# Kernel tuning notes

Measured on AMD Instinct MI355X. Metric: run time of the kernel, lower is better.

The kernel has to match this reference:

```python
import jax, jax.numpy as jnp
import numpy as np
from jax.scipy.special import logsumexp

WORD_DIM = 512
SCRF_DIM = 256
N_TAGS = 12
ALLOWED_SPAN = 8
START_ID = 10
STOP_ID = 11
SEQ_LEN = 768
N_SPANS = 96


def _compute_scores(h, Wl, bl, Wr, br, Gl, bgl, Gr, bgr, Wt, bt, transitions):
    # h: [1, L, D] already projected by Dense
    Lc, D = h.shape[1], h.shape[2]
    scores = jnp.zeros((1, Lc, Lc, D), h.dtype)
    diag = jnp.arange(Lc)
    ht = h
    scores = scores.at[:, diag, diag].set(ht)
    for sl in range(1, min(ALLOWED_SPAN, Lc)):
        l, r = ht[:, :-1], ht[:, 1:]
        h_hat = 4.0 * jax.nn.sigmoid(l @ Wl.T + bl + r @ Wr.T + br) - 2.0
        # exp/normalize over 3 gates == softmax over gate axis
        g = (l @ Gl.T + bgl + r @ Gr.T + bgr).reshape(1, Lc - sl, 3, D)
        wgt = jax.nn.softmax(g, axis=2)
        ht = wgt[:, :, 0] * h_hat + wgt[:, :, 1] * l + wgt[:, :, 2] * r
        scores = scores.at[:, diag[:Lc - sl], diag[sl:]].set(ht)
    tagsc = scores @ Wt.T + bt  # [1, L, L, T]
    # final[b,i,j,prev,tag] = tagsc[b,i,j,tag] + transitions[prev,tag]
    return tagsc[:, :, :, None, :] + transitions[None, None, None]


def _forward_pass(s5):
    # s5: [1, L, L, T, T]; semi-Markov forward algorithm, windows of width <= ALLOWED_SPAN
    Lc, T = s5.shape[1], s5.shape[3]
    A = ALLOWED_SPAN
    i0 = jnp.arange(1, Lc + 1)
    k = jnp.arange(A)
    p = i0[:, None] - A + k[None, :]              # candidate span-start positions [L, A]
    m = p >= 0                                    # valid window mask (istarts = max(0, i-A))
    x = s5[0][jnp.clip(p, 0), (i0 - 1)[:, None]]  # [L, A, T, T] span scores ending at i-1
    buf0 = jnp.full((A, T), -10000.0, s5.dtype).at[A - 1, START_ID].set(0.0)

    def step(buf, inp):
        xi, mi = inp
        # tmp[k, prev, tag] = score + logalpha[start, prev]
        tmp = jnp.where(mi[:, None, None], xi + buf[:, :, None], -1e30)
        na = logsumexp(tmp, axis=(0, 1))  # [T]
        return jnp.concatenate([buf[1:], na[None]], axis=0), na

    _, alphas = jax.lax.scan(step, buf0, (x, m))
    return alphas[-1, :STOP_ID].sum()


def _gold_score(s5, tags):
    Lc, T = s5.shape[1], s5.shape[3]
    gf = tags[:, :, 0] * (Lc * T * T) + tags[:, :, 1] * (T * T) + tags[:, :, 2] * T + tags[:, :, 3]
    return jnp.take_along_axis(s5.reshape(1, -1), gf, axis=1).sum()


def setup_inputs() -> dict:
    key = jax.random.key(0)
    ks = jax.random.split(key, 16)
    D, W3 = SCRF_DIM, 3 * SCRF_DIM
    s = 0.05
    def w(k, shape):
        return jax.random.normal(k, shape, dtype=jnp.float32) * s
    return {
        "feats": jax.random.normal(ks[0], (1, SEQ_LEN, WORD_DIM), dtype=jnp.float32),
        "tags": jax.random.randint(ks[1], (1, N_SPANS, 4), 0, N_TAGS),
        "Wd": w(ks[2], (D, WORD_DIM)), "bd": jnp.zeros((D,), jnp.float32),
        "Wl": w(ks[3], (D, D)), "bl": jnp.zeros((D,), jnp.float32),
        "Wr": w(ks[4], (D, D)), "br": jnp.zeros((D,), jnp.float32),
        "Gl": w(ks[5], (W3, D)), "bgl": jnp.zeros((W3,), jnp.float32),
        "Gr": w(ks[6], (W3, D)), "bgr": jnp.zeros((W3,), jnp.float32),
        "Wt": w(ks[7], (N_TAGS, D)), "bt": jnp.zeros((N_TAGS,), jnp.float32),
        "transitions": w(ks[8], (N_TAGS, N_TAGS)),
    }


def reference(feats, tags, Wd, bd, Wl, bl, Wr, br, Gl, bgl, Gr, bgr, Wt, bt, transitions):
    h = feats @ Wd.T + bd  # Dense: word_dim -> scrf_dim
    s5 = _compute_scores(h, Wl, bl, Wr, br, Gl, bgl, Gr, bgr, Wt, bt, transitions)
    gold = _gold_score(s5, tags)
    logZ = _forward_pass(s5)
    return logZ - gold
```

## Files before the change

### kernel.cpp

```cpp
#include <hip/hip_runtime.h>

typedef __attribute__((ext_vector_type(8))) short short8;
typedef __attribute__((ext_vector_type(4))) float f32x4;

__device__ __forceinline__ float bf2f(short s) {
  return __uint_as_float(((unsigned)(unsigned short)s) << 16);
}
__device__ __forceinline__ unsigned short f2bf(float f) {
  unsigned u = __float_as_uint(f);
  unsigned rounding = 0x7fffu + ((u >> 16) & 1u);
  return (unsigned short)((u + rounding) >> 16);
}

__global__ void prep_kernel(const float* __restrict__ feats, const float* __restrict__ Wd,
                            const float* __restrict__ Wl, const float* __restrict__ Wr,
                            const float* __restrict__ Gl, const float* __restrict__ Gr,
                            const float* __restrict__ bl, const float* __restrict__ br,
                            const float* __restrict__ bgl, const float* __restrict__ bgr,
                            unsigned short* __restrict__ featsB, unsigned short* __restrict__ WdB,
                            unsigned short* __restrict__ WcB, float* __restrict__ bc)
{
  int idx = blockIdx.x * 256 + threadIdx.x;
  if (idx < 393216) {
    featsB[idx] = f2bf(feats[idx]);
  } else if (idx < 524288) {
    int j = idx - 393216;
    WdB[j] = f2bf(Wd[j]);
  } else if (idx < 1048576) {
    int j = idx - 524288;
    int o = j >> 9, k = j & 511;
    float v;
    if (k < 256) v = (o < 256) ? Wl[o*256 + k] : Gl[(o-256)*256 + k];
    else { int k2 = k - 256; v = (o < 256) ? Wr[o*256 + k2] : Gr[(o-256)*256 + k2]; }
    WcB[j] = f2bf(v);
  } else if (idx < 1049600) {
    int o = idx - 1048576;
    bc[o] = (o < 256) ? bl[o] + br[o] : bgl[o-256] + bgr[o-256];
  }
}

__global__ __launch_bounds__(256) void hgemm_kernel(const unsigned short* __restrict__ A,
                                                    const unsigned short* __restrict__ W,
                                                    const float* __restrict__ bd,
                                                    unsigned short* __restrict__ C)
{
  __shared__ __align__(16) unsigned short As[64][72];
  __shared__ __align__(16) unsigned short Ws[64][72];
  int p0 = blockIdx.x * 64;
  int n0 = blockIdx.y * 64;
  int tid = threadIdx.x;
  int wave = tid >> 6, lane = tid & 63;
  f32x4 acc[4];
  #pragma unroll
  for (int i = 0; i < 4; ++i)
    #pragma unroll
    for (int j = 0; j < 4; ++j) acc[i][j] = 0.f;

  int lr = tid >> 3;
  int c8 = (tid & 7) * 8;
  for (int kt = 0; kt < 8; ++kt) {
    int kb = kt * 64;
    #pragma unroll
    for (int rr = 0; rr < 64; rr += 32) {
      int row = lr + rr;
      *(short8*)(&As[row][c8]) = *(const short8*)(A + (size_t)(p0 + row)*512 + kb + c8);
      *(short8*)(&Ws[row][c8]) = *(const short8*)(W + (size_t)(n0 + row)*512 + kb + c8);
    }
    __syncthreads();
    int q8 = (lane >> 4) * 8;
    #pragma unroll
    for (int kk = 0; kk < 2; ++kk) {
      short8 b = *(const short8*)(&Ws[wave*16 + (lane & 15)][kk*32 + q8]);
      #pragma unroll
      for (int mt = 0; mt < 4; ++mt) {
        short8 a = *(const short8*)(&As[mt*16 + (lane & 15)][kk*32 + q8]);
        acc[mt] = __builtin_amdgcn_mfma_f32_16x16x32_bf16(a, b, acc[mt], 0, 0, 0);
      }
    }
    __syncthreads();
  }
  int o = n0 + wave*16 + (lane & 15);
  float bias = bd[o];
  #pragma unroll
  for (int mt = 0; mt < 4; ++mt)
    #pragma unroll
    for (int r = 0; r < 4; ++r) {
      int row = p0 + mt*16 + (lane >> 4)*4 + r;
      C[row*256 + o] = f2bf(acc[mt][r] + bias);
    }
}

__global__ __launch_bounds__(256) void iter_kernel(const unsigned short* __restrict__ htp,
                                                   const unsigned short* __restrict__ Wc,
                                                   const float* __restrict__ bc,
                                                   unsigned short* __restrict__ htn,
                                                   int Mvalid)
{
  __shared__ __align__(16) unsigned short As[64][72];
  __shared__ __align__(16) unsigned short Ws[64][72];
  __shared__ float Cs[64][64];
  int p0 = blockIdx.x * 64;
  int n0 = blockIdx.y * 16;
  int tid = threadIdx.x;
  int wave = tid >> 6, lane = tid & 63;
  f32x4 acc[4];
  #pragma unroll
  for (int i = 0; i < 4; ++i)
    #pragma unroll
    for (int j = 0; j < 4; ++j) acc[i][j] = 0.f;

  int lr = tid >> 3;
  int c8 = (tid & 7) * 8;
  for (int kt = 0; kt < 8; ++kt) {
    int kb = kt * 64;
    int shift = kb >> 8;
    int kcol = kb & 255;
    #pragma unroll
    for (int rr = 0; rr < 64; rr += 32) {
      int row = lr + rr;
      int grow = p0 + row + shift; if (grow > 767) grow = 767;
      *(short8*)(&As[row][c8]) = *(const short8*)(htp + (size_t)grow*256 + kcol + c8);
      int o = (row >> 4)*256 + n0 + (row & 15);
      *(short8*)(&Ws[row][c8]) = *(const short8*)(Wc + (size_t)o*512 + kb + c8);
    }
    __syncthreads();
    int q8 = (lane >> 4) * 8;
    #pragma unroll
    for (int kk = 0; kk < 2; ++kk) {
      short8 b = *(const short8*)(&Ws[wave*16 + (lane & 15)][kk*32 + q8]);
      #pragma unroll
      for (int mt = 0; mt < 4; ++mt) {
        short8 a = *(const short8*)(&As[mt*16 + (lane & 15)][kk*32 + q8]);
        acc[mt] = __builtin_amdgcn_mfma_f32_16x16x32_bf16(a, b, acc[mt], 0, 0, 0);
      }
    }
    __syncthreads();
  }
  #pragma unroll
  for (int mt = 0; mt < 4; ++mt)
    #pragma unroll
    for (int r = 0; r < 4; ++r)
      Cs[mt*16 + (lane >> 4)*4 + r][wave*16 + (lane & 15)] = acc[mt][r];
  __syncthreads();

  int dl = tid & 15;
  int d = n0 + dl;
  float bz = bc[d], b0 = bc[256 + d], b1 = bc[512 + d], b2v = bc[768 + d];
  for (int pr = tid >> 4; pr < 64; pr += 16) {
    int p = p0 + pr;
    if (p >= Mvalid) continue;
    float z  = Cs[pr][dl]      + bz;
    float g0 = Cs[pr][16 + dl] + b0;
    float g1 = Cs[pr][32 + dl] + b1;
    float g2 = Cs[pr][48 + dl] + b2v;
    float l = bf2f((short)htp[p*256 + d]);
    float r = bf2f((short)htp[(p+1)*256 + d]);
    float hh = 4.f / (1.f + __expf(-z)) - 2.f;
    float mg = fmaxf(g0, fmaxf(g1, g2));
    float e0 = __expf(g0 - mg), e1 = __expf(g1 - mg), e2 = __expf(g2 - mg);
    float inv = 1.f / (e0 + e1 + e2);
    htn[p*256 + d] = f2bf((e0*hh + e1*l + e2*r) * inv);
  }
}

__global__ __launch_bounds__(128) void band_kernel(const unsigned short* __restrict__ htall,
                                                   const float* __restrict__ Wt,
                                                   const float* __restrict__ bt,
                                                   float* __restrict__ Bband,
                                                   float* __restrict__ Xn,
                                                   float* __restrict__ mu)
{
  __shared__ __align__(16) unsigned short rows[8][264];
  __shared__ float sred[96];
  __shared__ float smu;
  int i = blockIdx.x + 1;
  int tid = threadIdx.x;
  for (int q = tid; q < 256; q += 128) {
    int k = q >> 5, cc = (q & 31) * 8;
    int p = i - 8 + k, sl = 7 - k;
    short8 v;
    if (p >= 0) {
      v = *(const short8*)(htall + ((size_t)sl*768 + p)*256 + cc);
    } else {
      for (int j = 0; j < 8; ++j) v[j] = 0;
    }
    *(short8*)(&rows[k][cc]) = v;
  }
  __syncthreads();
  float res = -1e30f;
  if (tid < 96) {
    int t = tid >> 3, k = tid & 7;
    int p = i - 8 + k;
    if (p >= 0) {
      float acc = 0.f;
      for (int dch = 0; dch < 256; dch += 8) {
        float4 wa = *(const float4*)(Wt + t*256 + dch);
        float4 wb = *(const float4*)(Wt + t*256 + dch + 4);
        short8 hv = *(const short8*)(&rows[k][dch]);
        acc += wa.x*bf2f(hv[0]) + wa.y*bf2f(hv[1]) + wa.z*bf2f(hv[2]) + wa.w*bf2f(hv[3])
             + wb.x*bf2f(hv[4]) + wb.y*bf2f(hv[5]) + wb.z*bf2f(hv[6]) + wb.w*bf2f(hv[7]);
      }
      res = acc + bt[t];
    }
    Bband[(size_t)i*96 + tid] = res;
    sred[tid] = res;
  }
  __syncthreads();
  if (tid < 32) {
    float m = fmaxf(sred[tid], fmaxf(sred[tid+32], sred[tid+64]));
    #pragma unroll
    for (int off = 16; off; off >>= 1) m = fmaxf(m, __shfl_down(m, off));
    if (tid == 0) { mu[i] = m; smu = m; }
  }
  __syncthreads();
  if (tid < 96) Xn[(size_t)i*96 + tid] = __expf(res - smu);
}

__global__ __launch_bounds__(256) void chunkT_kernel(const float* __restrict__ Xn,
                                                     const float* __restrict__ mu,
                                                     const float* __restrict__ trans,
                                                     float* __restrict__ T,
                                                     float* __restrict__ C0)
{
  int chunk = blockIdx.y;
  int a = chunk * 16;
  int tid = threadIdx.x;
  if (blockIdx.x == 0 && tid == 0) C0[chunk] = 0.f;
  int wv = tid >> 6;
  int lane = tid & 63;
  int g = lane / 12;
  int t = lane - g * 12;
  int cidx = blockIdx.x * 20 + wv * 5 + g;
  bool active = (g < 5) && (cidx < 96);
  int c = active ? cidx : 95;
  int s = c / 12, tau = c - s * 12;
  float Etc[12];
  #pragma unroll
  for (int j = 0; j < 12; ++j) Etc[j] = __expf(trans[j*12 + t]);
  float NA[8], V[8];
  #pragma unroll
  for (int j = 0; j < 8; ++j) { NA[j] = 0.f; V[j] = 0.f; }
  #pragma unroll
  for (int j = 0; j < 8; ++j) if (j == s) {
    NA[j] = (t == tau) ? 1.f : 0.f;
    V[j]  = Etc[tau];
  }
  int gb = (g * 12) * 4;
  #pragma unroll
  for (int m = 1; m <= 16; ++m) {
    const float* xr = Xn + (size_t)(a + m) * 96 + t * 8;
    float4 x0 = *(const float4*)xr;
    float4 x1 = *(const float4*)(xr + 4);
    float sf = __expf(-mu[a + m]);
    float na = x0.x*V[0] + x0.y*V[1] + x0.z*V[2] + x0.w*V[3]
             + x1.x*V[4] + x1.y*V[5] + x1.z*V[6] + x1.w*V[7];
    int nai = __float_as_int(na);
    float nb[12];
    #pragma unroll
    for (int j = 0; j < 12; ++j)
      nb[j] = __int_as_float(__builtin_amdgcn_ds_bpermute(gb + j*4, nai));
    float p0 = nb[0]*Etc[0] + nb[1]*Etc[1] + nb[2]*Etc[2]  + nb[3]*Etc[3];
    float p1 = nb[4]*Etc[4] + nb[5]*Etc[5] + nb[6]*Etc[6]  + nb[7]*Etc[7];
    float p2 = nb[8]*Etc[8] + nb[9]*Etc[9] + nb[10]*Etc[10] + nb[11]*Etc[11];
    float v = (p0 + p1) + p2;
    #pragma unroll
    for (int k = 0; k < 7; ++k) { NA[k] = NA[k+1]*sf; V[k] = V[k+1]*sf; }
    NA[7] = na; V[7] = v;
  }
  if (active) {
    float* dst = T + (size_t)chunk * 9216 + c;
    #pragma unroll
    for (int j = 0; j < 8; ++j) dst[(size_t)(j*12 + t) * 96] = NA[j];
  }
}

#define TPAD 100
__global__ __launch_bounds__(256) void treemul_kernel(const float* __restrict__ Tin,
                                                      const float* __restrict__ Cin,
                                                      float* __restrict__ Tout,
                                                      float* __restrict__ Cout)
{
  __shared__ float Bs[96 * TPAD];
  __shared__ float Acs[96 * TPAD];
  __shared__ float red[8];
  int j = blockIdx.y;
  int cs = blockIdx.x * 48;
  const float* Ag = Tin + (size_t)(2*j) * 9216;
  const float* Bg = Tin + (size_t)(2*j + 1) * 9216;
  int tid = threadIdx.x;
  int wv = tid >> 6, lane = tid & 63;

  float4 av[9], bv[9];
  const float* ap = Ag + tid * 36;
  const float* bp = Bg + tid * 36;
  #pragma unroll
  for (int q = 0; q < 9; ++q) av[q] = *(const float4*)(ap + q*4);
  #pragma unroll
  for (int q = 0; q < 9; ++q) bv[q] = *(const float4*)(bp + q*4);
  float ma = 0.f, mb = 0.f;
  #pragma unroll
  for (int q = 0; q < 9; ++q) {
    ma = fmaxf(ma, fmaxf(fmaxf(av[q].x, av[q].y), fmaxf(av[q].z, av[q].w)));
    mb = fmaxf(mb, fmaxf(fmaxf(bv[q].x, bv[q].y), fmaxf(bv[q].z, bv[q].w)));
  }
  #pragma unroll
  for (int off = 32; off; off >>= 1) {
    ma = fmaxf(ma, __shfl_down(ma, off));
    mb = fmaxf(mb, __shfl_down(mb, off));
  }
  if (lane == 0) { red[wv] = ma; red[4 + wv] = mb; }
  __syncthreads();
  float fa = fmaxf(fmaxf(red[0], red[1]), fmaxf(red[2], red[3]));
  float fb = fmaxf(fmaxf(red[4], red[5]), fmaxf(red[6], red[7]));
  float ia = 1.0f / fa, ib = 1.0f / fb;

  #pragma unroll
  for (int q = 0; q < 9; ++q) {
    int e = tid*36 + q*4;
    int r = e / 96, k = e - r*96;
    float4 b = bv[q];
    b.x *= ib; b.y *= ib; b.z *= ib; b.w *= ib;
    *(float4*)&Bs[r*TPAD + k] = b;
    float4 a = av[q];
    Acs[(k+0)*TPAD + r] = a.x * ia;
    Acs[(k+1)*TPAD + r] = a.y * ia;
    Acs[(k+2)*TPAD + r] = a.z * ia;
    Acs[(k+3)*TPAD + r] = a.w * ia;
  }
  __syncthreads();

  int tr = tid >> 4, tc = tid & 15;
  int r0 = tr * 6, c0 = cs + tc * 3;
  float acc[6][3];
  #pragma unroll
  for (int i = 0; i < 6; ++i)
    #pragma unroll
    for (int m = 0; m < 3; ++m) acc[i][m] = 0.f;
  for (int k = 0; k < 96; k += 4) {
    float4 a0 = *(const float4*)&Acs[(c0+0)*TPAD + k];
    float4 a1 = *(const float4*)&Acs[(c0+1)*TPAD + k];
    float4 a2 = *(const float4*)&Acs[(c0+2)*TPAD + k];
    #pragma unroll
    for (int i = 0; i < 6; ++i) {
      float4 b = *(const float4*)&Bs[(r0+i)*TPAD + k];
      acc[i][0] += b.x*a0.x + b.y*a0.y + b.z*a0.z + b.w*a0.w;
      acc[i][1] += b.x*a1.x + b.y*a1.y + b.z*a1.z + b.w*a1.w;
      acc[i][2] += b.x*a2.x + b.y*a2.y + b.z*a2.z + b.w*a2.w;
    }
  }
  float* op = Tout + (size_t)j * 9216;
  #pragma unroll
  for (int i = 0; i < 6; ++i)
    #pragma unroll
    for (int m = 0; m < 3; ++m)
      op[(size_t)(r0+i)*96 + c0 + m] = acc[i][m];
  if (blockIdx.x == 0 && tid == 0)
    Cout[j] = Cin[2*j] + Cin[2*j + 1] + __logf(fa) + __logf(fb);
}

__global__ __launch_bounds__(256, 1) void final_kernel(const float* __restrict__ Tm,
    const float* __restrict__ Cm, const float* __restrict__ Bband,
    const float* __restrict__ mu, const float* __restrict__ trans,
    const float* __restrict__ bt, const int* __restrict__ tags,
    float* __restrict__ out)
{
  __shared__ float Qs[2][96 * TPAD];
  __shared__ float vv[4][96];
  __shared__ float red[8];
  __shared__ float redm[4];
  int tid = threadIdx.x;
  int wv = tid >> 6, lane = tid & 63;

  float4 P[9];
  const float* p0 = Tm + tid * 36;
  #pragma unroll
  for (int q = 0; q < 9; ++q) P[q] = *(const float4*)(p0 + q*4);

  float gold = 0.f;
  if (tid < 96) {
    int a = tags[tid*4+0], b = tags[tid*4+1], cc = tags[tid*4+2], d = tags[tid*4+3];
    float v = trans[cc*12 + d];
    int sl = b - a;
    if (sl >= 0 && sl < 8) v += Bband[(size_t)(b+1)*96 + d*8 + (7 - sl)];
    else v += bt[d];
    gold = v;
  }
  float mp = 0.f;
  for (int q = tid; q < 768; q += 256) mp += mu[1 + q];
  #pragma unroll
  for (int off = 32; off; off >>= 1) {
    gold += __shfl_down(gold, off);
    mp   += __shfl_down(mp, off);
  }
  if (lane == 0) { red[wv] = gold; red[4 + wv] = mp; }

  #pragma unroll
  for (int q = 0; q < 9; ++q) {
    int e = tid*36 + q*4;
    int r = e / 96, k = e - r*96;
    *(float4*)&Qs[0][r*TPAD + k] = P[q];
  }
  if (tid < 96) vv[0][tid] = (tid == 94) ? 1.f : 0.f;
  __syncthreads();
  float gold_t = red[0] + red[1] + red[2] + red[3];
  float musum  = red[4] + red[5] + red[6] + red[7];
  float Ct = Cm[0] + Cm[1] + Cm[2];

  #pragma unroll
  for (int s = 0; s < 3; ++s) {
    if (s < 2) {
      const float* pn = Tm + (size_t)(s+1)*9216 + tid*36;
      #pragma unroll
      for (int q = 0; q < 9; ++q) P[q] = *(const float4*)(pn + q*4);
    }
    float acc = 0.f;
    if (tid < 96) {
      const float* Qr = &Qs[s & 1][tid * TPAD];
      #pragma unroll
      for (int k = 0; k < 96; k += 4) {
        float4 qv = *(const float4*)(Qr + k);
        float4 zv = *(const float4*)&vv[s][k];
        acc += qv.x*zv.x + qv.y*zv.y + qv.z*zv.z + qv.w*zv.w;
      }
    }
    float am = (tid < 96) ? acc : 0.f;
    #pragma unroll
    for (int off = 32; off; off >>= 1) am = fmaxf(am, __shfl_down(am, off));
    if (lane == 0) redm[wv] = am;
    __syncthreads();
    float mx = fmaxf(fmaxf(redm[0], redm[1]), fmaxf(redm[2], redm[3]));
    Ct += __logf(mx);
    if (tid < 96) vv[s+1][tid] = acc / mx;
    if (s < 2) {
      #pragma unroll
      for (int q = 0; q < 9; ++q) {
        int e = tid*36 + q*4;
        int r = e / 96, k = e - r*96;
        *(float4*)&Qs[(s+1)&1][r*TPAD + k] = P[q];
      }
    }
    __syncthreads();
  }
  if (tid == 0) {
    float lsum = 0.f;
    #pragma unroll
    for (int t = 0; t < 11; ++t) lsum += __logf(vv[3][84 + t]);
    out[0] = lsum + 11.f * (Ct + musum) - gold_t;
  }
}

extern "C" void kernel_launch(void* const* d_in, const int* in_sizes, int n_in,
                              void* d_out, int out_size, void* d_ws, size_t ws_size,
                              hipStream_t stream)
{
  const float* feats = (const float*)d_in[0];
  const int*   tags  = (const int*)  d_in[1];
  const float* Wd    = (const float*)d_in[2];
  const float* bd    = (const float*)d_in[3];
  const float* Wl    = (const float*)d_in[4];
  const float* bl    = (const float*)d_in[5];
  const float* Wr    = (const float*)d_in[6];
  const float* br    = (const float*)d_in[7];
  const float* Gl    = (const float*)d_in[8];
  const float* bgl   = (const float*)d_in[9];
  const float* Gr    = (const float*)d_in[10];
  const float* bgr   = (const float*)d_in[11];
  const float* Wt    = (const float*)d_in[12];
  const float* bt    = (const float*)d_in[13];
  const float* trans = (const float*)d_in[14];
  float* out = (float*)d_out;

  char* ws = (char*)d_ws;
  unsigned short* featsB = (unsigned short*)(ws + 0);
  unsigned short* WdB    = (unsigned short*)(ws + 786432);
  unsigned short* WcB    = (unsigned short*)(ws + 1048576);
  float*          bc     = (float*)         (ws + 2097152);
  unsigned short* ht     = (unsigned short*)(ws + 2101248);
  float*          Bband  = (float*)         (ws + 5246976);
  float*          Xn     = (float*)         (ws + 5542272);
  float*          muv    = (float*)         (ws + 5837568);
  float*          T      = (float*)         (ws + 5841664);
  float*          Tb     = (float*)         (ws + 0);
  float*          C0     = (float*)         (ws + 1048576);
  float*          Ca     = (float*)         (ws + 1048832);
  float*          Cb     = (float*)         (ws + 1049088);

  prep_kernel<<<4100, 256, 0, stream>>>(feats, Wd, Wl, Wr, Gl, Gr, bl, br, bgl, bgr,
                                        featsB, WdB, WcB, bc);
  hgemm_kernel<<<dim3(12, 4), 256, 0, stream>>>(featsB, WdB, bd, ht);
  for (int sl = 1; sl <= 7; ++sl)
    iter_kernel<<<dim3(12, 16), 256, 0, stream>>>(ht + (size_t)(sl-1)*768*256, WcB, bc,
                                                  ht + (size_t)sl*768*256, 768 - sl);
  band_kernel<<<768, 128, 0, stream>>>(ht, Wt, bt, Bband, Xn, muv);
  chunkT_kernel<<<dim3(5, 48), 256, 0, stream>>>(Xn, muv, trans, T, C0);
  treemul_kernel<<<dim3(2, 24), 256, 0, stream>>>(T,  C0, Tb, Ca);
  treemul_kernel<<<dim3(2, 12), 256, 0, stream>>>(Tb, Ca, T,  Cb);
  treemul_kernel<<<dim3(2,  6), 256, 0, stream>>>(T,  Cb, Tb, Ca);
  treemul_kernel<<<dim3(2,  3), 256, 0, stream>>>(Tb, Ca, T,  Cb);
  final_kernel<<<1, 256, 0, stream>>>(T, Cb, Bband, muv, trans, bt, tags, out);
}
```

Baseline: 206.4 us.

## Fuse GEMM chain into cooperative kernel and merge band/chunk/tree stages

Replaces the prep, projection GEMM and seven iteration kernels with a single cooperative kernel. It converts fp32 inputs to bf16 on the fly and separates the span-length steps with grid syncs, which removes the separate conversion pass and eight launches. The band and chunk-transfer stages are merged into one kernel. The four-level tree reduction becomes two kernels that each combine four matrices, with per-matrix max scaling. The final kernel changes to two matrix-vector products. This cuts launch count and intermediate global traffic, but adds grid-sync overhead and converts the weights redundantly in every iteration.

```diff
diff --git a/kernel.cpp b/kernel.cpp
--- a/kernel.cpp
+++ b/kernel.cpp
@@ -1,4 +1,6 @@
 #include <hip/hip_runtime.h>
+#include <hip/hip_cooperative_groups.h>
+namespace cg = cooperative_groups;
 
 typedef __attribute__((ext_vector_type(8))) short short8;
 typedef __attribute__((ext_vector_type(4))) float f32x4;
@@ -11,370 +13,473 @@
   unsigned rounding = 0x7fffu + ((u >> 16) & 1u);
   return (unsigned short)((u + rounding) >> 16);
 }
-
-__global__ void prep_kernel(const float* __restrict__ feats, const float* __restrict__ Wd,
-                            const float* __restrict__ Wl, const float* __restrict__ Wr,
-                            const float* __restrict__ Gl, const float* __restrict__ Gr,
-                            const float* __restrict__ bl, const float* __restrict__ br,
-                            const float* __restrict__ bgl, const float* __restrict__ bgr,
-                            unsigned short* __restrict__ featsB, unsigned short* __restrict__ WdB,
-                            unsigned short* __restrict__ WcB, float* __restrict__ bc)
-{
-  int idx = blockIdx.x * 256 + threadIdx.x;
-  if (idx < 393216) {
-    featsB[idx] = f2bf(feats[idx]);
-  } else if (idx < 524288) {
-    int j = idx - 393216;
-    WdB[j] = f2bf(Wd[j]);
-  } else if (idx < 1048576) {
-    int j = idx - 524288;
-    int o = j >> 9, k = j & 511;
-    float v;
-    if (k < 256) v = (o < 256) ? Wl[o*256 + k] : Gl[(o-256)*256 + k];
-    else { int k2 = k - 256; v = (o < 256) ? Wr[o*256 + k2] : Gr[(o-256)*256 + k2]; }
-    WcB[j] = f2bf(v);
-  } else if (idx < 1049600) {
-    int o = idx - 1048576;
-    bc[o] = (o < 256) ? bl[o] + br[o] : bgl[o-256] + bgr[o-256];
-  }
-}
-
-__global__ __launch_bounds__(256) void hgemm_kernel(const unsigned short* __restrict__ A,
-                                                    const unsigned short* __restrict__ W,
-                                                    const float* __restrict__ bd,
-                                                    unsigned short* __restrict__ C)
-{
-  __shared__ __align__(16) unsigned short As[64][72];
-  __shared__ __align__(16) unsigned short Ws[64][72];
-  int p0 = blockIdx.x * 64;
-  int n0 = blockIdx.y * 64;
-  int tid = threadIdx.x;
-  int wave = tid >> 6, lane = tid & 63;
-  f32x4 acc[4];
-  #pragma unroll
-  for (int i = 0; i < 4; ++i)
-    #pragma unroll
-    for (int j = 0; j < 4; ++j) acc[i][j] = 0.f;
-
-  int lr = tid >> 3;
-  int c8 = (tid & 7) * 8;
-  for (int kt = 0; kt < 8; ++kt) {
-    int kb = kt * 64;
-    #pragma unroll
-    for (int rr = 0; rr < 64; rr += 32) {
-      int row = lr + rr;
-      *(short8*)(&As[row][c8]) = *(const short8*)(A + (size_t)(p0 + row)*512 + kb + c8);
-      *(short8*)(&Ws[row][c8]) = *(const short8*)(W + (size_t)(n0 + row)*512 + kb + c8);
-    }
-    __syncthreads();
-    int q8 = (lane >> 4) * 8;
-    #pragma unroll
-    for (int kk = 0; kk < 2; ++kk) {
-      short8 b = *(const short8*)(&Ws[wave*16 + (lane & 15)][kk*32 + q8]);
-      #pragma unroll
-      for (int mt = 0; mt < 4; ++mt) {
-        short8 a = *(const short8*)(&As[mt*16 + (lane & 15)][kk*32 + q8]);
-        acc[mt] = __builtin_amdgcn_mfma_f32_16x16x32_bf16(a, b, acc[mt], 0, 0, 0);
-      }
-    }
-    __syncthreads();
-  }
-  int o = n0 + wave*16 + (lane & 15);
-  float bias = bd[o];
-  #pragma unroll
-  for (int mt = 0; mt < 4; ++mt)
-    #pragma unroll
-    for (int r = 0; r < 4; ++r) {
-      int row = p0 + mt*16 + (lane >> 4)*4 + r;
-      C[row*256 + o] = f2bf(acc[mt][r] + bias);
-    }
-}
-
-__global__ __launch_bounds__(256) void iter_kernel(const unsigned short* __restrict__ htp,
-                                                   const unsigned short* __restrict__ Wc,
-                                                   const float* __restrict__ bc,
-                                                   unsigned short* __restrict__ htn,
-                                                   int Mvalid)
-{
+__device__ __forceinline__ short8 cvt8(float4 a, float4 b) {
+  short8 r;
+  r[0]=(short)f2bf(a.x); r[1]=(short)f2bf(a.y); r[2]=(short)f2bf(a.z); r[3]=(short)f2bf(a.w);
+  r[4]=(short)f2bf(b.x); r[5]=(short)f2bf(b.y); r[6]=(short)f2bf(b.z); r[7]=(short)f2bf(b.w);
+  return r;
+}
+
+__global__ __launch_bounds__(256) void gemm_chain_kernel(
+    const float* __restrict__ feats, const float* __restrict__ Wd, const float* __restrict__ bd,
+    const float* __restrict__ Wl, const float* __restrict__ bl,
+    const float* __restrict__ Wr, const float* __restrict__ br,
+    const float* __restrict__ Gl, const float* __restrict__ bgl,
+    const float* __restrict__ Gr, const float* __restrict__ bgr,
+    unsigned short* __restrict__ ht)
+{
+  cg::grid_group grid = cg::this_grid();
   __shared__ __align__(16) unsigned short As[64][72];
   __shared__ __align__(16) unsigned short Ws[64][72];
   __shared__ float Cs[64][64];
-  int p0 = blockIdx.x * 64;
-  int n0 = blockIdx.y * 16;
   int tid = threadIdx.x;
   int wave = tid >> 6, lane = tid & 63;
-  f32x4 acc[4];
-  #pragma unroll
-  for (int i = 0; i < 4; ++i)
-    #pragma unroll
-    for (int j = 0; j < 4; ++j) acc[i][j] = 0.f;
-
   int lr = tid >> 3;
   int c8 = (tid & 7) * 8;
-  for (int kt = 0; kt < 8; ++kt) {
-    int kb = kt * 64;
-    int shift = kb >> 8;
-    int kcol = kb & 255;
-    #pragma unroll
-    for (int rr = 0; rr < 64; rr += 32) {
-      int row = lr + rr;
-      int grow = p0 + row + shift; if (grow > 767) grow = 767;
-      *(short8*)(&As[row][c8]) = *(const short8*)(htp + (size_t)grow*256 + kcol + c8);
-      int o = (row >> 4)*256 + n0 + (row & 15);
-      *(short8*)(&Ws[row][c8]) = *(const short8*)(Wc + (size_t)o*512 + kb + c8);
-    }
-    __syncthreads();
-    int q8 = (lane >> 4) * 8;
-    #pragma unroll
-    for (int kk = 0; kk < 2; ++kk) {
-      short8 b = *(const short8*)(&Ws[wave*16 + (lane & 15)][kk*32 + q8]);
-      #pragma unroll
-      for (int mt = 0; mt < 4; ++mt) {
-        short8 a = *(const short8*)(&As[mt*16 + (lane & 15)][kk*32 + q8]);
-        acc[mt] = __builtin_amdgcn_mfma_f32_16x16x32_bf16(a, b, acc[mt], 0, 0, 0);
-      }
-    }
-    __syncthreads();
-  }
-  #pragma unroll
-  for (int mt = 0; mt < 4; ++mt)
-    #pragma unroll
-    for (int r = 0; r < 4; ++r)
-      Cs[mt*16 + (lane >> 4)*4 + r][wave*16 + (lane & 15)] = acc[mt][r];
-  __syncthreads();
-
+
+  if (blockIdx.x < 48) {
+    int p0 = (blockIdx.x % 12) * 64;
+    int n0 = (blockIdx.x / 12) * 64;
+    f32x4 acc[4];
+    #pragma unroll
+    for (int i = 0; i < 4; ++i)
+      #pragma unroll
+      for (int j = 0; j < 4; ++j) acc[i][j] = 0.f;
+    for (int kt = 0; kt < 8; ++kt) {
+      int kb = kt * 64;
+      #pragma unroll
+      for (int rr = 0; rr < 64; rr += 32) {
+        int row = lr + rr;
+        const float* fp = feats + (size_t)(p0 + row)*512 + kb + c8;
+        *(short8*)(&As[row][c8]) = cvt8(*(const float4*)fp, *(const float4*)(fp + 4));
+        const float* wp = Wd + (size_t)(n0 + row)*512 + kb + c8;
+        *(short8*)(&Ws[row][c8]) = cvt8(*(const float4*)wp, *(const float4*)(wp + 4));
+      }
+      __syncthreads();
+      int q8 = (lane >> 4) * 8;
+      #pragma unroll
+      for (int kk = 0; kk < 2; ++kk) {
+        short8 b = *(const short8*)(&Ws[wave*16 + (lane & 15)][kk*32 + q8]);
+        #pragma unroll
+        for (int mt = 0; mt < 4; ++mt) {
+          short8 a = *(const short8*)(&As[mt*16 + (lane & 15)][kk*32 + q8]);
+          acc[mt] = __builtin_amdgcn_mfma_f32_16x16x32_bf16(a, b, acc[mt], 0, 0, 0);
+        }
+      }
+      __syncthreads();
+    }
+    int o = n0 + wave*16 + (lane & 15);
+    float bias = bd[o];
+    #pragma unroll
+    for (int mt = 0; mt < 4; ++mt)
+      #pragma unroll
+      for (int r = 0; r < 4; ++r) {
+        int row = p0 + mt*16 + (lane >> 4)*4 + r;
+        ht[(size_t)row*256 + o] = f2bf(acc[mt][r] + bias);
+      }
+  }
+  __threadfence();
+  grid.sync();
+
+  int p0 = (blockIdx.x % 12) * 64;
+  int n0 = (blockIdx.x / 12) * 16;
   int dl = tid & 15;
   int d = n0 + dl;
-  float bz = bc[d], b0 = bc[256 + d], b1 = bc[512 + d], b2v = bc[768 + d];
-  for (int pr = tid >> 4; pr < 64; pr += 16) {
-    int p = p0 + pr;
-    if (p >= Mvalid) continue;
-    float z  = Cs[pr][dl]      + bz;
-    float g0 = Cs[pr][16 + dl] + b0;
-    float g1 = Cs[pr][32 + dl] + b1;
-    float g2 = Cs[pr][48 + dl] + b2v;
-    float l = bf2f((short)htp[p*256 + d]);
-    float r = bf2f((short)htp[(p+1)*256 + d]);
-    float hh = 4.f / (1.f + __expf(-z)) - 2.f;
-    float mg = fmaxf(g0, fmaxf(g1, g2));
-    float e0 = __expf(g0 - mg), e1 = __expf(g1 - mg), e2 = __expf(g2 - mg);
-    float inv = 1.f / (e0 + e1 + e2);
-    htn[p*256 + d] = f2bf((e0*hh + e1*l + e2*r) * inv);
-  }
-}
-
-__global__ __launch_bounds__(128) void band_kernel(const unsigned short* __restrict__ htall,
-                                                   const float* __restrict__ Wt,
-                                                   const float* __restrict__ bt,
-                                                   float* __restrict__ Bband,
-                                                   float* __restrict__ Xn,
-                                                   float* __restrict__ mu)
-{
-  __shared__ __align__(16) unsigned short rows[8][264];
-  __shared__ float sred[96];
-  __shared__ float smu;
-  int i = blockIdx.x + 1;
+  float bz  = bl[d] + br[d];
+  float b0  = bgl[d] + bgr[d];
+  float b1  = bgl[256 + d] + bgr[256 + d];
+  float b2v = bgl[512 + d] + bgr[512 + d];
+
+  for (int sl = 1; sl <= 7; ++sl) {
+    const unsigned short* htp = ht + (size_t)(sl-1)*196608;
+    unsigned short* htn = ht + (size_t)sl*196608;
+    int Mvalid = 768 - sl;
+    f32x4 acc[4];
+    #pragma unroll
+    for (int i = 0; i < 4; ++i)
+      #pragma unroll
+      for (int j = 0; j < 4; ++j) acc[i][j] = 0.f;
+    for (int kt = 0; kt < 8; ++kt) {
+      int kb = kt * 64;
+      int shift = kb >> 8;
+      int kcol = kb & 255;
+      #pragma unroll
+      for (int rr = 0; rr < 64; rr += 32) {
+        int row = lr + rr;
+        int grow = p0 + row + shift; if (grow > 767) grow = 767;
+        *(short8*)(&As[row][c8]) = *(const short8*)(htp + (size_t)grow*256 + kcol + c8);
+        int seg = row >> 4;
+        int orow = n0 + (row & 15);
+        const float* wsrc;
+        if (kt < 4) wsrc = (seg == 0) ? (Wl + (size_t)orow*256 + kb + c8)
+                                      : (Gl + ((size_t)(seg-1)*256 + orow)*256 + kb + c8);
+        else        wsrc = (seg == 0) ? (Wr + (size_t)orow*256 + (kb - 256) + c8)
+                                      : (Gr + ((size_t)(seg-1)*256 + orow)*256 + (kb - 256) + c8);
+        *(short8*)(&Ws[row][c8]) = cvt8(*(const float4*)wsrc, *(const float4*)(wsrc + 4));
+      }
+      __syncthreads();
+      int q8 = (lane >> 4) * 8;
+      #pragma unroll
+      for (int kk = 0; kk < 2; ++kk) {
+        short8 b = *(const short8*)(&Ws[wave*16 + (lane & 15)][kk*32 + q8]);
+        #pragma unroll
+        for (int mt = 0; mt < 4; ++mt) {
+          short8 a = *(const short8*)(&As[mt*16 + (lane & 15)][kk*32 + q8]);
+          acc[mt] = __builtin_amdgcn_mfma_f32_16x16x32_bf16(a, b, acc[mt], 0, 0, 0);
+        }
+      }
+      __syncthreads();
+    }
+    #pragma unroll
+    for (int mt = 0; mt < 4; ++mt)
+      #pragma unroll
+      for (int r = 0; r < 4; ++r)
+        Cs[mt*16 + (lane >> 4)*4 + r][wave*16 + (lane & 15)] = acc[mt][r];
+    __syncthreads();
+    for (int pr = tid >> 4; pr < 64; pr += 16) {
+      int p = p0 + pr;
+      if (p < Mvalid) {
+        float z  = Cs[pr][dl]      + bz;
+        float g0 = Cs[pr][16 + dl] + b0;
+        float g1 = Cs[pr][32 + dl] + b1;
+        float g2 = Cs[pr][48 + dl] + b2v;
+        float l = bf2f((short)htp[(size_t)p*256 + d]);
+        float r = bf2f((short)htp[(size_t)(p+1)*256 + d]);
+        float hh = 4.f / (1.f + __expf(-z)) - 2.f;
+        float mg = fmaxf(g0, fmaxf(g1, g2));
+        float e0 = __expf(g0 - mg), e1 = __expf(g1 - mg), e2 = __expf(g2 - mg);
+        htn[(size_t)p*256 + d] = f2bf((e0*hh + e1*l + e2*r) / (e0 + e1 + e2));
+      }
+    }
+    __threadfence();
+    grid.sync();
+  }
+}
+
+#define HPAD 264
+__global__ __launch_bounds__(256) void bandchunk_kernel(
+    const unsigned short* __restrict__ htall, const float* __restrict__ Wt,
+    const float* __restrict__ bt, const float* __restrict__ trans,
+    float* __restrict__ Bband, float* __restrict__ mug,
+    float* __restrict__ T, float* __restrict__ Tmax)
+{
+  __shared__ __align__(16) unsigned short hrow[8][16][HPAD];
+  __shared__ __align__(16) float Wts[3072];
+  __shared__ float Bls[16][100];
+  __shared__ float Xls[16][100];
+  __shared__ float muls[16], sfs[16];
+  __shared__ float redmax[4];
+  int c = blockIdx.x;
+  int a = c * 16;
   int tid = threadIdx.x;
-  for (int q = tid; q < 256; q += 128) {
-    int k = q >> 5, cc = (q & 31) * 8;
-    int p = i - 8 + k, sl = 7 - k;
+
+  for (int q = tid; q < 4096; q += 256) {
+    int sl = q >> 9;
+    int rem = q & 511;
+    int j = rem >> 5;
+    int cc = (rem & 31) * 8;
+    int p = a - sl + j;
     short8 v;
-    if (p >= 0) {
-      v = *(const short8*)(htall + ((size_t)sl*768 + p)*256 + cc);
-    } else {
-      for (int j = 0; j < 8; ++j) v[j] = 0;
-    }
-    *(short8*)(&rows[k][cc]) = v;
-  }
-  __syncthreads();
-  float res = -1e30f;
-  if (tid < 96) {
-    int t = tid >> 3, k = tid & 7;
-    int p = i - 8 + k;
+    if (p >= 0) v = *(const short8*)(htall + ((size_t)sl*768 + p)*256 + cc);
+    else { for (int x = 0; x < 8; ++x) v[x] = 0; }
+    *(short8*)(&hrow[sl][j][cc]) = v;
+  }
+  for (int q = tid; q < 3072; q += 256) Wts[q] = Wt[q];
+  __syncthreads();
+
+  #pragma unroll
+  for (int rep = 0; rep < 6; ++rep) {
+    int idx = rep * 256 + tid;
+    int j = idx / 96, col = idx - j * 96;
+    int t = col >> 3, k = col & 7, sl = 7 - k;
+    int p = a - sl + j;
+    float res = -1e30f;
     if (p >= 0) {
       float acc = 0.f;
+      const unsigned short* hr = &hrow[sl][j][0];
+      const float* wr = &Wts[t * 256];
       for (int dch = 0; dch < 256; dch += 8) {
-        float4 wa = *(const float4*)(Wt + t*256 + dch);
-        float4 wb = *(const float4*)(Wt + t*256 + dch + 4);
-        short8 hv = *(const short8*)(&rows[k][dch]);
+        short8 hv = *(const short8*)(hr + dch);
+        float4 wa = *(const float4*)(wr + dch);
+        float4 wb = *(const float4*)(wr + dch + 4);
         acc += wa.x*bf2f(hv[0]) + wa.y*bf2f(hv[1]) + wa.z*bf2f(hv[2]) + wa.w*bf2f(hv[3])
              + wb.x*bf2f(hv[4]) + wb.y*bf2f(hv[5]) + wb.z*bf2f(hv[6]) + wb.w*bf2f(hv[7]);
       }
       res = acc + bt[t];
     }
-    Bband[(size_t)i*96 + tid] = res;
-    sred[tid] = res;
-  }
-  __syncthreads();
-  if (tid < 32) {
-    float m = fmaxf(sred[tid], fmaxf(sred[tid+32], sred[tid+64]));
-    #pragma unroll
-    for (int off = 16; off; off >>= 1) m = fmaxf(m, __shfl_down(m, off));
-    if (tid == 0) { mu[i] = m; smu = m; }
-  }
-  __syncthreads();
-  if (tid < 96) Xn[(size_t)i*96 + tid] = __expf(res - smu);
-}
-
-__global__ __launch_bounds__(256) void chunkT_kernel(const float* __restrict__ Xn,
-                                                     const float* __restrict__ mu,
-                                                     const float* __restrict__ trans,
-                                                     float* __restrict__ T,
-                                                     float* __restrict__ C0)
-{
-  int chunk = blockIdx.y;
-  int a = chunk * 16;
-  int tid = threadIdx.x;
-  if (blockIdx.x == 0 && tid == 0) C0[chunk] = 0.f;
-  int wv = tid >> 6;
-  int lane = tid & 63;
+    Bls[j][col] = res;
+  }
+  __syncthreads();
+  if (tid < 16) {
+    float m = -1e30f;
+    for (int col = 0; col < 96; ++col) m = fmaxf(m, Bls[tid][col]);
+    muls[tid] = m;
+    sfs[tid] = __expf(-m);
+    mug[a + 1 + tid] = m;
+  }
+  __syncthreads();
+  #pragma unroll
+  for (int rep = 0; rep < 6; ++rep) {
+    int idx = rep * 256 + tid;
+    int j = idx / 96, col = idx - j * 96;
+    float b = Bls[j][col];
+    Bband[(size_t)(a + 1 + j) * 96 + col] = b;
+    Xls[j][col] = __expf(b - muls[j]);
+  }
+  __syncthreads();
+
+  int wv = tid >> 6, lane = tid & 63;
   int g = lane / 12;
   int t = lane - g * 12;
-  int cidx = blockIdx.x * 20 + wv * 5 + g;
-  bool active = (g < 5) && (cidx < 96);
-  int c = active ? cidx : 95;
-  int s = c / 12, tau = c - s * 12;
   float Etc[12];
   #pragma unroll
   for (int j = 0; j < 12; ++j) Etc[j] = __expf(trans[j*12 + t]);
-  float NA[8], V[8];
-  #pragma unroll
-  for (int j = 0; j < 8; ++j) { NA[j] = 0.f; V[j] = 0.f; }
-  #pragma unroll
-  for (int j = 0; j < 8; ++j) if (j == s) {
-    NA[j] = (t == tau) ? 1.f : 0.f;
-    V[j]  = Etc[tau];
-  }
   int gb = (g * 12) * 4;
-  #pragma unroll
-  for (int m = 1; m <= 16; ++m) {
-    const float* xr = Xn + (size_t)(a + m) * 96 + t * 8;
-    float4 x0 = *(const float4*)xr;
-    float4 x1 = *(const float4*)(xr + 4);
-    float sf = __expf(-mu[a + m]);
-    float na = x0.x*V[0] + x0.y*V[1] + x0.z*V[2] + x0.w*V[3]
-             + x1.x*V[4] + x1.y*V[5] + x1.z*V[6] + x1.w*V[7];
-    int nai = __float_as_int(na);
-    float nb[12];
-    #pragma unroll
-    for (int j = 0; j < 12; ++j)
-      nb[j] = __int_as_float(__builtin_amdgcn_ds_bpermute(gb + j*4, nai));
-    float p0 = nb[0]*Etc[0] + nb[1]*Etc[1] + nb[2]*Etc[2]  + nb[3]*Etc[3];
-    float p1 = nb[4]*Etc[4] + nb[5]*Etc[5] + nb[6]*Etc[6]  + nb[7]*Etc[7];
-    float p2 = nb[8]*Etc[8] + nb[9]*Etc[9] + nb[10]*Etc[10] + nb[11]*Etc[11];
-    float v = (p0 + p1) + p2;
-    #pragma unroll
-    for (int k = 0; k < 7; ++k) { NA[k] = NA[k+1]*sf; V[k] = V[k+1]*sf; }
-    NA[7] = na; V[7] = v;
-  }
-  if (active) {
-    float* dst = T + (size_t)chunk * 9216 + c;
-    #pragma unroll
-    for (int j = 0; j < 8; ++j) dst[(size_t)(j*12 + t) * 96] = NA[j];
-  }
-}
-
-#define TPAD 100
-__global__ __launch_bounds__(256) void treemul_kernel(const float* __restrict__ Tin,
-                                                      const float* __restrict__ Cin,
-                                                      float* __restrict__ Tout,
-                                                      float* __restrict__ Cout)
-{
-  __shared__ float Bs[96 * TPAD];
-  __shared__ float Acs[96 * TPAD];
-  __shared__ float red[8];
-  int j = blockIdx.y;
-  int cs = blockIdx.x * 48;
-  const float* Ag = Tin + (size_t)(2*j) * 9216;
-  const float* Bg = Tin + (size_t)(2*j + 1) * 9216;
+  float tmax = 0.f;
+  for (int pass = 0; pass < 5; ++pass) {
+    int cidx = pass * 20 + wv * 5 + g;
+    bool act = (g < 5) && (cidx < 96);
+    int cc2 = act ? cidx : 95;
+    int s = cc2 / 12, tau = cc2 - s * 12;
+    float NA[8], V[8];
+    #pragma unroll
+    for (int j = 0; j < 8; ++j) { NA[j] = 0.f; V[j] = 0.f; }
+    #pragma unroll
+    for (int j = 0; j < 8; ++j) if (j == s) {
+      NA[j] = (t == tau) ? 1.f : 0.f;
+      V[j]  = Etc[tau];
+    }
+    #pragma unroll
+    for (int m = 1; m <= 16; ++m) {
+      int jj = m - 1;
+      const float* xr = &Xls[jj][t * 8];
+      float4 x0 = *(const float4*)xr;
+      float4 x1 = *(const float4*)(xr + 4);
+      float sf = sfs[jj];
+      float na = x0.x*V[0] + x0.y*V[1] + x0.z*V[2] + x0.w*V[3]
+               + x1.x*V[4] + x1.y*V[5] + x1.z*V[6] + x1.w*V[7];
+      int nai = __float_as_int(na);
+      float nb[12];
+      #pragma unroll
+      for (int j = 0; j < 12; ++j)
+        nb[j] = __int_as_float(__builtin_amdgcn_ds_bpermute(gb + j*4, nai));
+      float p0 = nb[0]*Etc[0] + nb[1]*Etc[1] + nb[2]*Etc[2]  + nb[3]*Etc[3];
+      float p1 = nb[4]*Etc[4] + nb[5]*Etc[5] + nb[6]*Etc[6]  + nb[7]*Etc[7];
+      float p2 = nb[8]*Etc[8] + nb[9]*Etc[9] + nb[10]*Etc[10] + nb[11]*Etc[11];
+      float v = (p0 + p1) + p2;
+      #pragma unroll
+      for (int k = 0; k < 7; ++k) { NA[k] = NA[k+1]*sf; V[k] = V[k+1]*sf; }
+      NA[7] = na; V[7] = v;
+    }
+    if (act) {
+      float* dst = T + (size_t)c * 9216 + cidx;
+      #pragma unroll
+      for (int j = 0; j < 8; ++j) {
+        dst[(size_t)(j*12 + t) * 96] = NA[j];
+        tmax = fmaxf(tmax, NA[j]);
+      }
+    }
+  }
+  #pragma unroll
+  for (int off = 32; off; off >>= 1) tmax = fmaxf(tmax, __shfl_down(tmax, off));
+  if (lane == 0) redmax[wv] = tmax;
+  __syncthreads();
+  if (tid == 0)
+    Tmax[c] = fmaxf(fmaxf(fmaxf(redmax[0], redmax[1]), fmaxf(redmax[2], redmax[3])), 1e-30f);
+}
+
+#define TP 100
+__device__ __forceinline__ void mm_acc(const float* __restrict__ Bs,
+                                       const float* __restrict__ Ain,
+                                       int r0, int cl0, float acc[6][3])
+{
+  #pragma unroll
+  for (int i = 0; i < 6; ++i)
+    #pragma unroll
+    for (int m = 0; m < 3; ++m) acc[i][m] = 0.f;
+  for (int k = 0; k < 96; k += 4) {
+    float4 a0 = *(const float4*)(Ain + (cl0+0)*TP + k);
+    float4 a1 = *(const float4*)(Ain + (cl0+1)*TP + k);
+    float4 a2 = *(const float4*)(Ain + (cl0+2)*TP + k);
+    #pragma unroll
+    for (int i = 0; i < 6; ++i) {
+      float4 b = *(const float4*)(Bs + (r0+i)*TP + k);
+      acc[i][0] += b.x*a0.x + b.y*a0.y + b.z*a0.z + b.w*a0.w;
+      acc[i][1] += b.x*a1.x + b.y*a1.y + b.z*a1.z + b.w*a1.w;
+      acc[i][2] += b.x*a2.x + b.y*a2.y + b.z*a2.z + b.w*a2.w;
+    }
+  }
+}
+
+__global__ __launch_bounds__(256) void tree1_kernel(const float* __restrict__ Tin,
+    const float* __restrict__ Tmax, float* __restrict__ Tout,
+    float* __restrict__ TmaxO, float* __restrict__ Cout)
+{
+  __shared__ float Bs[96 * TP];
+  __shared__ float Rt[2][48 * TP];
+  __shared__ float redm[4];
+  int j = blockIdx.x >> 1, slice = blockIdx.x & 1;
+  int c0 = slice * 48;
   int tid = threadIdx.x;
-  int wv = tid >> 6, lane = tid & 63;
-
-  float4 av[9], bv[9];
-  const float* ap = Ag + tid * 36;
-  const float* bp = Bg + tid * 36;
-  #pragma unroll
-  for (int q = 0; q < 9; ++q) av[q] = *(const float4*)(ap + q*4);
-  #pragma unroll
-  for (int q = 0; q < 9; ++q) bv[q] = *(const float4*)(bp + q*4);
-  float ma = 0.f, mb = 0.f;
-  #pragma unroll
-  for (int q = 0; q < 9; ++q) {
-    ma = fmaxf(ma, fmaxf(fmaxf(av[q].x, av[q].y), fmaxf(av[q].z, av[q].w)));
-    mb = fmaxf(mb, fmaxf(fmaxf(bv[q].x, bv[q].y), fmaxf(bv[q].z, bv[q].w)));
-  }
-  #pragma unroll
-  for (int off = 32; off; off >>= 1) {
-    ma = fmaxf(ma, __shfl_down(ma, off));
-    mb = fmaxf(mb, __shfl_down(mb, off));
-  }
-  if (lane == 0) { red[wv] = ma; red[4 + wv] = mb; }
-  __syncthreads();
-  float fa = fmaxf(fmaxf(red[0], red[1]), fmaxf(red[2], red[3]));
-  float fb = fmaxf(fmaxf(red[4], red[5]), fmaxf(red[6], red[7]));
-  float ia = 1.0f / fa, ib = 1.0f / fb;
-
+  const float* M0 = Tin + (size_t)(4*j    ) * 9216;
+  const float* M1 = Tin + (size_t)(4*j + 1) * 9216;
+  const float* M2 = Tin + (size_t)(4*j + 2) * 9216;
+  const float* M3 = Tin + (size_t)(4*j + 3) * 9216;
+  float m0 = Tmax[4*j], m1 = Tmax[4*j+1], m2 = Tmax[4*j+2], m3 = Tmax[4*j+3];
+  float i0 = 1.f/m0, i1 = 1.f/m1, i2 = 1.f/m2, i3 = 1.f/m3;
+
+  for (int q = tid; q < 4608; q += 256) {
+    int k = q / 48, cc = q - k*48;
+    Rt[0][cc*TP + k] = M0[(size_t)k*96 + c0 + cc] * i0;
+  }
+  for (int q = tid; q < 9216; q += 256) {
+    int r = q / 96, k = q - r*96;
+    Bs[r*TP + k] = M1[q] * i1;
+  }
+  __syncthreads();
+  int r0 = (tid >> 4) * 6, cl0 = (tid & 15) * 3;
+  float acc[6][3];
+  float4 p[9];
+  #pragma unroll
+  for (int q = 0; q < 9; ++q) p[q] = *(const float4*)(M2 + tid*36 + q*4);
+  mm_acc(Bs, Rt[0], r0, cl0, acc);
+  #pragma unroll
+  for (int i = 0; i < 6; ++i)
+    #pragma unroll
+    for (int m = 0; m < 3; ++m) Rt[1][(cl0+m)*TP + (r0+i)] = acc[i][m];
+  __syncthreads();
   #pragma unroll
   for (int q = 0; q < 9; ++q) {
     int e = tid*36 + q*4;
     int r = e / 96, k = e - r*96;
-    float4 b = bv[q];
-    b.x *= ib; b.y *= ib; b.z *= ib; b.w *= ib;
-    *(float4*)&Bs[r*TPAD + k] = b;
-    float4 a = av[q];
-    Acs[(k+0)*TPAD + r] = a.x * ia;
-    Acs[(k+1)*TPAD + r] = a.y * ia;
-    Acs[(k+2)*TPAD + r] = a.z * ia;
-    Acs[(k+3)*TPAD + r] = a.w * ia;
-  }
-  __syncthreads();
-
-  int tr = tid >> 4, tc = tid & 15;
-  int r0 = tr * 6, c0 = cs + tc * 3;
+    float4 v = p[q]; v.x *= i2; v.y *= i2; v.z *= i2; v.w *= i2;
+    *(float4*)&Bs[r*TP + k] = v;
+  }
+  #pragma unroll
+  for (int q = 0; q < 9; ++q) p[q] = *(const float4*)(M3 + tid*36 + q*4);
+  __syncthreads();
+  mm_acc(Bs, Rt[1], r0, cl0, acc);
+  #pragma unroll
+  for (int i = 0; i < 6; ++i)
+    #pragma unroll
+    for (int m = 0; m < 3; ++m) Rt[0][(cl0+m)*TP + (r0+i)] = acc[i][m];
+  __syncthreads();
+  #pragma unroll
+  for (int q = 0; q < 9; ++q) {
+    int e = tid*36 + q*4;
+    int r = e / 96, k = e - r*96;
+    float4 v = p[q]; v.x *= i3; v.y *= i3; v.z *= i3; v.w *= i3;
+    *(float4*)&Bs[r*TP + k] = v;
+  }
+  __syncthreads();
+  mm_acc(Bs, Rt[0], r0, cl0, acc);
+  float* op = Tout + (size_t)j * 9216;
+  float mx = 0.f;
+  #pragma unroll
+  for (int i = 0; i < 6; ++i)
+    #pragma unroll
+    for (int m = 0; m < 3; ++m) {
+      float v = acc[i][m];
+      op[(size_t)(r0+i)*96 + c0 + cl0 + m] = v;
+      mx = fmaxf(mx, v);
+    }
+  int wv = tid >> 6, lane = tid & 63;
+  #pragma unroll
+  for (int off = 32; off; off >>= 1) mx = fmaxf(mx, __shfl_down(mx, off));
+  if (lane == 0) redm[wv] = mx;
+  __syncthreads();
+  if (tid == 0)
+    TmaxO[blockIdx.x] = fmaxf(fmaxf(fmaxf(redm[0], redm[1]), fmaxf(redm[2], redm[3])), 1e-30f);
+  if (slice == 0 && tid == 0)
+    Cout[j] = __logf(m0) + __logf(m1) + __logf(m2) + __logf(m3);
+}
+
+__global__ __launch_bounds__(256) void tree2_kernel(const float* __restrict__ Tin,
+    const float* __restrict__ TmaxI, const float* __restrict__ Cin,
+    float* __restrict__ Tout, float* __restrict__ Cout)
+{
+  __shared__ float Bs[96 * TP];
+  __shared__ float Rt[2][48 * TP];
+  int j = blockIdx.x >> 1, slice = blockIdx.x & 1;
+  int c0 = slice * 48;
+  int tid = threadIdx.x;
+  const float* M0 = Tin + (size_t)(4*j    ) * 9216;
+  const float* M1 = Tin + (size_t)(4*j + 1) * 9216;
+  const float* M2 = Tin + (size_t)(4*j + 2) * 9216;
+  const float* M3 = Tin + (size_t)(4*j + 3) * 9216;
+  float m0 = fmaxf(TmaxI[2*(4*j  )], TmaxI[2*(4*j  )+1]);
+  float m1 = fmaxf(TmaxI[2*(4*j+1)], TmaxI[2*(4*j+1)+1]);
+  float m2 = fmaxf(TmaxI[2*(4*j+2)], TmaxI[2*(4*j+2)+1]);
+  float m3 = fmaxf(TmaxI[2*(4*j+3)], TmaxI[2*(4*j+3)+1]);
+  float i0 = 1.f/m0, i1 = 1.f/m1, i2 = 1.f/m2, i3 = 1.f/m3;
+
+  for (int q = tid; q < 4608; q += 256) {
+    int k = q / 48, cc = q - k*48;
+    Rt[0][cc*TP + k] = M0[(size_t)k*96 + c0 + cc] * i0;
+  }
+  for (int q = tid; q < 9216; q += 256) {
+    int r = q / 96, k = q - r*96;
+    Bs[r*TP + k] = M1[q] * i1;
+  }
+  __syncthreads();
+  int r0 = (tid >> 4) * 6, cl0 = (tid & 15) * 3;
   float acc[6][3];
-  #pragma unroll
-  for (int i = 0; i < 6; ++i)
-    #pragma unroll
-    for (int m = 0; m < 3; ++m) acc[i][m] = 0.f;
-  for (int k = 0; k < 96; k += 4) {
-    float4 a0 = *(const float4*)&Acs[(c0+0)*TPAD + k];
-    float4 a1 = *(const float4*)&Acs[(c0+1)*TPAD + k];
-    float4 a2 = *(const float4*)&Acs[(c0+2)*TPAD + k];
-    #pragma unroll
-    for (int i = 0; i < 6; ++i) {
-      float4 b = *(const float4*)&Bs[(r0+i)*TPAD + k];
-      acc[i][0] += b.x*a0.x + b.y*a0.y + b.z*a0.z + b.w*a0.w;
-      acc[i][1] += b.x*a1.x + b.y*a1.y + b.z*a1.z + b.w*a1.w;
-      acc[i][2] += b.x*a2.x + b.y*a2.y + b.z*a2.z + b.w*a2.w;
-    }
-  }
+  float4 p[9];
+  #pragma unroll
+  for (int q = 0; q < 9; ++q) p[q] = *(const float4*)(M2 + tid*36 + q*4);
+  mm_acc(Bs, Rt[0], r0, cl0, acc);
+  #pragma unroll
+  for (int i = 0; i < 6; ++i)
+    #pragma unroll
+    for (int m = 0; m < 3; ++m) Rt[1][(cl0+m)*TP + (r0+i)] = acc[i][m];
+  __syncthreads();
+  #pragma unroll
+  for (int q = 0; q < 9; ++q) {
+    int e = tid*36 + q*4;
+    int r = e / 96, k = e - r*96;
+    float4 v = p[q]; v.x *= i2; v.y *= i2; v.z *= i2; v.w *= i2;
+    *(float4*)&Bs[r*TP + k] = v;
+  }
+  #pragma unroll
+  for (int q = 0; q < 9; ++q) p[q] = *(const float4*)(M3 + tid*36 + q*4);
+  __syncthreads();
+  mm_acc(Bs, Rt[1], r0, cl0, acc);
+  #pragma unroll
+  for (int i = 0; i < 6; ++i)
+    #pragma unroll
+    for (int m = 0; m < 3; ++m) Rt[0][(cl0+m)*TP + (r0+i)] = acc[i][m];
+  __syncthreads();
+  #pragma unroll
+  for (int q = 0; q < 9; ++q) {
+    int e = tid*36 + q*4;
+    int r = e / 96, k = e - r*96;
+    float4 v = p[q]; v.x *= i3; v.y *= i3; v.z *= i3; v.w *= i3;
+    *(float4*)&Bs[r*TP + k] = v;
+  }
+  __syncthreads();
+  mm_acc(Bs, Rt[0], r0, cl0, acc);
   float* op = Tout + (size_t)j * 9216;
   #pragma unroll
   for (int i = 0; i < 6; ++i)
     #pragma unroll
     for (int m = 0; m < 3; ++m)
-      op[(size_t)(r0+i)*96 + c0 + m] = acc[i][m];
-  if (blockIdx.x == 0 && tid == 0)
-    Cout[j] = Cin[2*j] + Cin[2*j + 1] + __logf(fa) + __logf(fb);
-}
-
-__global__ __launch_bounds__(256, 1) void final_kernel(const float* __restrict__ Tm,
-    const float* __restrict__ Cm, const float* __restrict__ Bband,
-    const float* __restrict__ mu, const float* __restrict__ trans,
+      op[(size_t)(r0+i)*96 + c0 + cl0 + m] = acc[i][m];
+  if (slice == 0 && tid == 0)
+    Cout[j] = Cin[4*j] + Cin[4*j+1] + Cin[4*j+2] + Cin[4*j+3]
+            + __logf(m0) + __logf(m1) + __logf(m2) + __logf(m3);
+}
+
+__global__ __launch_bounds__(256, 1) void final_kernel(const float* __restrict__ Tc,
+    const float* __restrict__ Cb, const float* __restrict__ Bband,
+    const float* __restrict__ mug, const float* __restrict__ trans,
     const float* __restrict__ bt, const int* __restrict__ tags,
     float* __restrict__ out)
 {
-  __shared__ float Qs[2][96 * TPAD];
-  __shared__ float vv[4][96];
+  __shared__ float Qs[96 * TP];
+  __shared__ float v1[96], v2[96], v3[96];
   __shared__ float red[8];
-  __shared__ float redm[4];
   int tid = threadIdx.x;
   int wv = tid >> 6, lane = tid & 63;
-
-  float4 P[9];
-  const float* p0 = Tm + tid * 36;
-  #pragma unroll
-  for (int q = 0; q < 9; ++q) P[q] = *(const float4*)(p0 + q*4);
 
   float gold = 0.f;
   if (tid < 96) {
@@ -386,66 +491,51 @@
     gold = v;
   }
   float mp = 0.f;
-  for (int q = tid; q < 768; q += 256) mp += mu[1 + q];
+  for (int q = tid; q < 768; q += 256) mp += mug[1 + q];
   #pragma unroll
   for (int off = 32; off; off >>= 1) {
     gold += __shfl_down(gold, off);
     mp   += __shfl_down(mp, off);
   }
   if (lane == 0) { red[wv] = gold; red[4 + wv] = mp; }
-
-  #pragma unroll
-  for (int q = 0; q < 9; ++q) {
-    int e = tid*36 + q*4;
-    int r = e / 96, k = e - r*96;
-    *(float4*)&Qs[0][r*TPAD + k] = P[q];
-  }
-  if (tid < 96) vv[0][tid] = (tid == 94) ? 1.f : 0.f;
-  __syncthreads();
-  float gold_t = red[0] + red[1] + red[2] + red[3];
-  float musum  = red[4] + red[5] + red[6] + red[7];
-  float Ct = Cm[0] + Cm[1] + Cm[2];
-
-  #pragma unroll
-  for (int s = 0; s < 3; ++s) {
-    if (s < 2) {
-      const float* pn = Tm + (size_t)(s+1)*9216 + tid*36;
-      #pragma unroll
-      for (int q = 0; q < 9; ++q) P[q] = *(const float4*)(pn + q*4);
-    }
-    float acc = 0.f;
-    if (tid < 96) {
-      const float* Qr = &Qs[s & 1][tid * TPAD];
-      #pragma unroll
-      for (int k = 0; k < 96; k += 4) {
-        float4 qv = *(const float4*)(Qr + k);
-        float4 zv = *(const float4*)&vv[s][k];
-        acc += qv.x*zv.x + qv.y*zv.y + qv.z*zv.z + qv.w*zv.w;
-      }
-    }
-    float am = (tid < 96) ? acc : 0.f;
-    #pragma unroll
-    for (int off = 32; off; off >>= 1) am = fmaxf(am, __shfl_down(am, off));
-    if (lane == 0) redm[wv] = am;
-    __syncthreads();
-    float mx = fmaxf(fmaxf(redm[0], redm[1]), fmaxf(redm[2], redm[3]));
-    Ct += __logf(mx);
-    if (tid < 96) vv[s+1][tid] = acc / mx;
-    if (s < 2) {
-      #pragma unroll
-      for (int q = 0; q < 9; ++q) {
-        int e = tid*36 + q*4;
-        int r = e / 96, k = e - r*96;
-        *(float4*)&Qs[(s+1)&1][r*TPAD + k] = P[q];
-      }
-    }
-    __syncthreads();
-  }
+  if (tid < 96) v1[tid] = Tc[(size_t)tid*96 + 94];
+  for (int q = tid; q < 9216; q += 256) {
+    int r = q / 96, k = q - r*96;
+    Qs[r*TP + k] = Tc[9216 + q];
+  }
+  __syncthreads();
+  float goldt = red[0] + red[1] + red[2] + red[3];
+  float musum = red[4] + red[5] + red[6] + red[7];
+  if (tid < 96) {
+    float a = 0.f;
+    for (int k = 0; k < 96; k += 4) {
+      float4 qv = *(const float4*)&Qs[tid*TP + k];
+      float4 zv = *(const float4*)&v1[k];
+      a += qv.x*zv.x + qv.y*zv.y + qv.z*zv.z + qv.w*zv.w;
+    }
+    v2[tid] = a;
+  }
+  __syncthreads();
+  for (int q = tid; q < 9216; q += 256) {
+    int r = q / 96, k = q - r*96;
+    Qs[r*TP + k] = Tc[18432 + q];
+  }
+  __syncthreads();
+  if (tid < 96) {
+    float a = 0.f;
+    for (int k = 0; k < 96; k += 4) {
+      float4 qv = *(const float4*)&Qs[tid*TP + k];
+      float4 zv = *(const float4*)&v2[k];
+      a += qv.x*zv.x + qv.y*zv.y + qv.z*zv.z + qv.w*zv.w;
+    }
+    v3[tid] = a;
+  }
+  __syncthreads();
   if (tid == 0) {
-    float lsum = 0.f;
-    #pragma unroll
-    for (int t = 0; t < 11; ++t) lsum += __logf(vv[3][84 + t]);
-    out[0] = lsum + 11.f * (Ct + musum) - gold_t;
+    float ls = 0.f;
+    #pragma unroll
+    for (int t = 0; t < 11; ++t) ls += __logf(v3[84 + t]);
+    out[0] = ls + 11.f * (Cb[0] + Cb[1] + Cb[2] + musum) - goldt;
   }
 }
 
@@ -471,31 +561,23 @@
   float* out = (float*)d_out;
 
   char* ws = (char*)d_ws;
-  unsigned short* featsB = (unsigned short*)(ws + 0);
-  unsigned short* WdB    = (unsigned short*)(ws + 786432);
-  unsigned short* WcB    = (unsigned short*)(ws + 1048576);
-  float*          bc     = (float*)         (ws + 2097152);
-  unsigned short* ht     = (unsigned short*)(ws + 2101248);
-  float*          Bband  = (float*)         (ws + 5246976);
-  float*          Xn     = (float*)         (ws + 5542272);
-  float*          muv    = (float*)         (ws + 5837568);
-  float*          T      = (float*)         (ws + 5841664);
-  float*          Tb     = (float*)         (ws + 0);
-  float*          C0     = (float*)         (ws + 1048576);
-  float*          Ca     = (float*)         (ws + 1048832);
-  float*          Cb     = (float*)         (ws + 1049088);
-
-  prep_kernel<<<4100, 256, 0, stream>>>(feats, Wd, Wl, Wr, Gl, Gr, bl, br, bgl, bgr,
-                                        featsB, WdB, WcB, bc);
-  hgemm_kernel<<<dim3(12, 4), 256, 0, stream>>>(featsB, WdB, bd, ht);
-  for (int sl = 1; sl <= 7; ++sl)
-    iter_kernel<<<dim3(12, 16), 256, 0, stream>>>(ht + (size_t)(sl-1)*768*256, WcB, bc,
-                                                  ht + (size_t)sl*768*256, 768 - sl);
-  band_kernel<<<768, 128, 0, stream>>>(ht, Wt, bt, Bband, Xn, muv);
-  chunkT_kernel<<<dim3(5, 48), 256, 0, stream>>>(Xn, muv, trans, T, C0);
-  treemul_kernel<<<dim3(2, 24), 256, 0, stream>>>(T,  C0, Tb, Ca);
-  treemul_kernel<<<dim3(2, 12), 256, 0, stream>>>(Tb, Ca, T,  Cb);
-  treemul_kernel<<<dim3(2,  6), 256, 0, stream>>>(T,  Cb, Tb, Ca);
-  treemul_kernel<<<dim3(2,  3), 256, 0, stream>>>(Tb, Ca, T,  Cb);
-  final_kernel<<<1, 256, 0, stream>>>(T, Cb, Bband, muv, trans, bt, tags, out);
-}
+  unsigned short* ht    = (unsigned short*)(ws + 0);
+  float*          Bband = (float*)(ws + 3145728);
+  float*          mug   = (float*)(ws + 3441024);
+  float*          T     = (float*)(ws + 3444224);
+  float*          Tb    = (float*)(ws + 5213696);
+  float*          Tc    = (float*)(ws + 5656064);
+  float*          Tmax  = (float*)(ws + 5766656);
+  float*          Tmax1 = (float*)(ws + 5766848);
+  float*          Ca    = (float*)(ws + 5766944);
+  float*          Cb    = (float*)(ws + 5766992);
+
+  void* cargs[] = {(void*)&feats, (void*)&Wd, (void*)&bd, (void*)&Wl, (void*)&bl,
+                   (void*)&Wr, (void*)&br, (void*)&Gl, (void*)&bgl, (void*)&Gr,
+                   (void*)&bgr, (void*)&ht};
+  hipLaunchCooperativeKernel((void*)gemm_chain_kernel, dim3(192), dim3(256), cargs, 0, stream);
+  bandchunk_kernel<<<48, 256, 0, stream>>>(ht, Wt, bt, trans, Bband, mug, T, Tmax);
+  tree1_kernel<<<24, 256, 0, stream>>>(T, Tmax, Tb, Tmax1, Ca);
+  tree2_kernel<<<6, 256, 0, stream>>>(Tb, Tmax1, Ca, Tc, Cb);
+  final_kernel<<<1, 256, 0, stream>>>(Tc, Cb, Bband, mug, trans, bt, tags, out);
+}
```

After: 598.0 us. 2.9x slower.
